# Optimization experiments

Measured on AMD Instinct MI355X. Metric: run time of the kernel, lower is better.

## Reference

```python
import jax, jax.numpy as jnp
import numpy as np
import math

N_HEAD = 16

def _rope_tables(seq, dh, dtype):
    inv_freq = 1.0 / (10000.0 ** (jnp.arange(0, dh, 2, dtype=jnp.float32) / dh))
    angle = jnp.arange(seq, dtype=jnp.float32)[:, None] * inv_freq[None, :]  # [S, dh/2]
    sin = jnp.repeat(jnp.sin(angle), 2, axis=-1).astype(dtype)  # [S, dh]
    cos = jnp.repeat(jnp.cos(angle), 2, axis=-1).astype(dtype)
    return sin, cos

def _rotate_half(x):
    x_even = x[..., ::2]
    x_odd = x[..., 1::2]
    return jnp.stack([-x_odd, x_even], axis=-1).reshape(x.shape)

def _apply_rope(x, sin, cos):
    # x: [B, H, S, dh]; sin/cos: [S, dh]
    return x * cos[None, None] + _rotate_half(x) * sin[None, None]

def setup_inputs() -> dict:
    key = jax.random.key(0)
    ks = jax.random.split(key, 9)
    B, S, D = 2, 2048, 2048
    scale = 1.0 / math.sqrt(D)
    x = jax.random.normal(ks[0], (B, S, D), dtype=jnp.float32)
    wq = jax.random.normal(ks[1], (D, D), dtype=jnp.float32) * scale
    wk = jax.random.normal(ks[2], (D, D), dtype=jnp.float32) * scale
    wv = jax.random.normal(ks[3], (D, D), dtype=jnp.float32) * scale
    wo = jax.random.normal(ks[4], (D, D), dtype=jnp.float32) * scale
    bq = jnp.zeros((D,), jnp.float32)
    bk = jnp.zeros((D,), jnp.float32)
    bv = jnp.zeros((D,), jnp.float32)
    bo = jnp.zeros((D,), jnp.float32)
    # causal mask: True = masked (strict upper triangle)
    mask = jnp.triu(jnp.ones((S, S), dtype=bool), k=1)[None, None]  # [1,1,S,S]
    return {"x": x, "wq": wq, "bq": bq, "wk": wk, "bk": bk, "wv": wv, "bv": bv,
            "wo": wo, "bo": bo, "mask": mask}

def reference(x, wq, bq, wk, bk, wv, bv, wo, bo, mask):
    B, S, D = x.shape
    H = N_HEAD
    dh = D // H
    # projections (torch Linear: x @ W.T + b)
    q = (x @ wq.T + bq).reshape(B, S, H, dh).transpose(0, 2, 1, 3)  # [B,H,S,dh]
    k = (x @ wk.T + bk).reshape(B, S, H, dh).transpose(0, 2, 1, 3)
    v = (x @ wv.T + bv).reshape(B, S, H, dh).transpose(0, 2, 1, 3)
    sin, cos = _rope_tables(S, dh, x.dtype)
    q = _apply_rope(q, sin, cos)
    k = _apply_rope(k, sin, cos)
    scores = jnp.einsum('bhqd,bhkd->bhqk', q, k) / math.sqrt(dh)
    scores = jnp.where(mask, -jnp.inf, scores)
    attn = jax.nn.softmax(scores, axis=-1)
    attn = jnp.nan_to_num(attn, nan=0.0)
    out = jnp.einsum('bhqk,bhkd->bhqd', attn, v)  # [B,H,S,dh]
    out = out.transpose(0, 2, 1, 3).reshape(B, S, D)
    return out @ wo.T + bo
```

## Files before the change

### kernel.cpp

```cpp
#include <hip/hip_runtime.h>
#include <math.h>


typedef _Float16 half8 __attribute__((ext_vector_type(8)));
typedef _Float16 half4v __attribute__((ext_vector_type(4)));
typedef float f32x4 __attribute__((ext_vector_type(4)));

__device__ __forceinline__ void gl_lds16(const void* g, void* l) {
  __builtin_amdgcn_global_load_lds(
      (const __attribute__((address_space(1))) unsigned int*)g,
      (__attribute__((address_space(3))) unsigned int*)l, 16, 0, 0);
}

__global__ void cast_f32_f16(const float* __restrict__ src, _Float16* __restrict__ dst, int n4) {
  int i = blockIdx.x * blockDim.x + threadIdx.x;
  if (i >= n4) return;
  float4 v = reinterpret_cast<const float4*>(src)[i];
  half4v o;
  o[0] = (_Float16)v.x; o[1] = (_Float16)v.y; o[2] = (_Float16)v.z; o[3] = (_Float16)v.w;
  reinterpret_cast<half4v*>(dst)[i] = o;
}

__global__ void cast_w(const float* __restrict__ w0, const float* __restrict__ w1,
                       const float* __restrict__ w2, const float* __restrict__ w3,
                       _Float16* __restrict__ wdst) {
  const float* s = blockIdx.y == 0 ? w0 : blockIdx.y == 1 ? w1 : blockIdx.y == 2 ? w2 : w3;
  int i = blockIdx.x * blockDim.x + threadIdx.x;
  float4 v = reinterpret_cast<const float4*>(s)[i];
  half4v o;
  o[0] = (_Float16)v.x; o[1] = (_Float16)v.y; o[2] = (_Float16)v.z; o[3] = (_Float16)v.w;
  reinterpret_cast<half4v*>(wdst)[(size_t)blockIdx.y * 1048576 + i] = o;
}

template <bool OUT_F32>
__global__ __launch_bounds__(512, 2) void gemm_bt256(
    const _Float16* __restrict__ A,
    const _Float16* __restrict__ B,
    const float* __restrict__ b0, const float* __restrict__ b1,
    const float* __restrict__ b2,
    void* __restrict__ Cout,
    int M, int N, int K) {
  __shared__ _Float16 As[2][16384];
  __shared__ _Float16 Bs[2][16384];
  const int bm = blockIdx.y * 256, bn = blockIdx.x * 256;
  const int tid = threadIdx.x;
  const int wave = tid >> 6, lane = tid & 63;
  const int quad = lane >> 4, l16 = lane & 15;
  const int wm = (wave >> 2) * 128, wn = (wave & 3) * 64;

  const int srow = tid >> 3;
  const int sx = (tid & 7) ^ (srow & 7);
  const _Float16* Ag = A + (size_t)(bm + srow) * K + sx * 8;
  const _Float16* Bg[4];
#pragma unroll
  for (int c = 0; c < 4; ++c) {
    int r = (((c * 2 + (srow >> 5)) & 3) << 6) + ((c >> 1) << 5) + (srow & 31);
    Bg[c] = B + (size_t)(bn + r) * K + sx * 8;
  }

#define STAGE_A(buf, R, kt) \
  gl_lds16(Ag + (size_t)(R) * K + (kt) * 64, &As[buf][(R) * 64 + tid * 8])
#define STAGE_B(buf, c, kt) \
  gl_lds16(Bg[c] + (kt) * 64, &Bs[buf][(c) * 4096 + tid * 8])

  const int axor = l16 & 7;
  const int sl0 = ((0 + quad) ^ axor) * 8;
  const int sl1 = ((4 + quad) ^ axor) * 8;
  const int aoff = (wm + l16) * 64;
  const int q4 = (wn >> 6) * 32;

#define RD_A(i, kk) \
  (*reinterpret_cast<const half8*>(&As[cur][aoff + (i) * 1024 + ((kk) ? sl1 : sl0)]))
#define RD_B(j, kk) \
  (*reinterpret_cast<const half8*>( \
      &Bs[cur][((((j) >> 1) * 128 + q4 + ((j) & 1) * 16 + l16)) * 64 + ((kk) ? sl1 : sl0)]))

  f32x4 acc[8][4];
#pragma unroll
  for (int i = 0; i < 8; ++i)
#pragma unroll
    for (int j = 0; j < 4; ++j) acc[i][j] = f32x4{0.f, 0.f, 0.f, 0.f};

  half8 a[4][2], b[4][2];
  const int NT = K >> 6;

  STAGE_A(0, 0, 0); STAGE_A(0, 128, 0);
  STAGE_B(0, 0, 0); STAGE_B(0, 1, 0);
  STAGE_B(0, 2, 0); STAGE_B(0, 3, 0);
  STAGE_A(0, 64, 0); STAGE_A(0, 192, 0);
  if (NT > 1) {
    STAGE_A(1, 0, 1); STAGE_A(1, 128, 1);
    STAGE_B(1, 0, 1); STAGE_B(1, 1, 1);
    STAGE_B(1, 2, 1); STAGE_B(1, 3, 1);
    asm volatile("s_waitcnt vmcnt(6)");
  } else {
    asm volatile("s_waitcnt vmcnt(0)");
  }
  __builtin_amdgcn_s_barrier();

  for (int t = 0; t < NT; ++t) {
    const int cur = t & 1, nxt = cur ^ 1;
    const bool pf1 = (t + 1 < NT);
    const bool pf2 = (t + 2 < NT);

#pragma unroll
    for (int i = 0; i < 4; ++i) {
      a[i][0] = RD_A(i, 0); a[i][1] = RD_A(i, 1);
    }
#pragma unroll
    for (int j = 0; j < 2; ++j) {
      b[j][0] = RD_B(j, 0); b[j][1] = RD_B(j, 1);
    }
    if (pf1) { STAGE_A(nxt, 64, t + 1); STAGE_A(nxt, 192, t + 1); }
    __builtin_amdgcn_s_barrier();
    __builtin_amdgcn_s_setprio(1);
#pragma unroll
    for (int i = 0; i < 4; ++i)
#pragma unroll
      for (int j = 0; j < 2; ++j) {
        acc[i][j] = __builtin_amdgcn_mfma_f32_16x16x32_f16(a[i][0], b[j][0], acc[i][j], 0, 0, 0);
        acc[i][j] = __builtin_amdgcn_mfma_f32_16x16x32_f16(a[i][1], b[j][1], acc[i][j], 0, 0, 0);
      }
    __builtin_amdgcn_s_setprio(0);
    __builtin_amdgcn_s_barrier();

#pragma unroll
    for (int j = 2; j < 4; ++j) {
      b[j][0] = RD_B(j, 0); b[j][1] = RD_B(j, 1);
    }
    if (pf2) { STAGE_A(cur, 0, t + 2); STAGE_A(cur, 128, t + 2); }
    __builtin_amdgcn_s_barrier();
    __builtin_amdgcn_s_setprio(1);
#pragma unroll
    for (int i = 0; i < 4; ++i)
#pragma unroll
      for (int j = 2; j < 4; ++j) {
        acc[i][j] = __builtin_amdgcn_mfma_f32_16x16x32_f16(a[i][0], b[j][0], acc[i][j], 0, 0, 0);
        acc[i][j] = __builtin_amdgcn_mfma_f32_16x16x32_f16(a[i][1], b[j][1], acc[i][j], 0, 0, 0);
      }
    __builtin_amdgcn_s_setprio(0);
    __builtin_amdgcn_s_barrier();

#pragma unroll
    for (int i = 0; i < 4; ++i) {
      a[i][0] = RD_A(i + 4, 0); a[i][1] = RD_A(i + 4, 1);
    }
    if (pf2) { STAGE_B(cur, 0, t + 2); STAGE_B(cur, 1, t + 2); }
    __builtin_amdgcn_s_barrier();
    __builtin_amdgcn_s_setprio(1);
#pragma unroll
    for (int i = 0; i < 4; ++i)
#pragma unroll
      for (int j = 0; j < 2; ++j) {
        acc[i + 4][j] = __builtin_amdgcn_mfma_f32_16x16x32_f16(a[i][0], b[j][0], acc[i + 4][j], 0, 0, 0);
        acc[i + 4][j] = __builtin_amdgcn_mfma_f32_16x16x32_f16(a[i][1], b[j][1], acc[i + 4][j], 0, 0, 0);
      }
    __builtin_amdgcn_s_setprio(0);
    __builtin_amdgcn_s_barrier();

    if (pf2) { STAGE_B(cur, 2, t + 2); STAGE_B(cur, 3, t + 2); }
    __builtin_amdgcn_s_barrier();
    __builtin_amdgcn_s_setprio(1);
#pragma unroll
    for (int i = 0; i < 4; ++i)
#pragma unroll
      for (int j = 2; j < 4; ++j) {
        acc[i + 4][j] = __builtin_amdgcn_mfma_f32_16x16x32_f16(a[i][0], b[j][0], acc[i + 4][j], 0, 0, 0);
        acc[i + 4][j] = __builtin_amdgcn_mfma_f32_16x16x32_f16(a[i][1], b[j][1], acc[i + 4][j], 0, 0, 0);
      }
    __builtin_amdgcn_s_setprio(0);
    if (pf2)
      asm volatile("s_waitcnt vmcnt(6)");
    else
      asm volatile("s_waitcnt vmcnt(0)");
    __builtin_amdgcn_s_barrier();
  }

#pragma unroll
  for (int j = 0; j < 4; ++j) {
    const int gc = bn + wn + j * 16 + l16;
    const float* bp = (gc < 2048) ? b0 : (gc < 4096 ? b1 : b2);
    const float bz = bp[gc & 2047];
#pragma unroll
    for (int i = 0; i < 8; ++i) {
#pragma unroll
      for (int r = 0; r < 4; ++r) {
        const int gr = bm + wm + i * 16 + quad * 4 + r;
        float v = acc[i][j][r] + bz;
        if (OUT_F32)
          reinterpret_cast<float*>(Cout)[(size_t)gr * N + gc] = v;
        else
          reinterpret_cast<_Float16*>(Cout)[(size_t)gr * N + gc] = (_Float16)v;
      }
    }
  }
#undef STAGE_A
#undef STAGE_B
#undef RD_A
#undef RD_B
}

template <bool OUT_F32>
__global__ __launch_bounds__(512, 2) void gemm_btn128(
    const _Float16* __restrict__ A,
    const _Float16* __restrict__ B,
    const float* __restrict__ bias,
    void* __restrict__ Cout,
    int M, int N, int K) {
  __shared__ _Float16 As[2][16384];
  __shared__ _Float16 Bs[2][8192];
  const int bm = blockIdx.y * 256, bn = blockIdx.x * 128;
  const int tid = threadIdx.x;
  const int wave = tid >> 6, lane = tid & 63;
  const int quad = lane >> 4, l16 = lane & 15;
  const int wm = (wave >> 2) * 128, wq = wave & 3;

  const int srow = tid >> 3;
  const int sx = (tid & 7) ^ (srow & 7);
  const _Float16* Ag = A + (size_t)(bm + srow) * K + sx * 8;
  const _Float16* Bg[2];
#pragma unroll
  for (int c = 0; c < 2; ++c)
    Bg[c] = B + (size_t)(bn + (srow >> 4) * 32 + c * 16 + (srow & 15)) * K + sx * 8;

#define STAGE_A(buf, R, kt) \
  gl_lds16(Ag + (size_t)(R) * K + (kt) * 64, &As[buf][(R) * 64 + tid * 8])
#define STAGE_B(buf, c, kt) \
  gl_lds16(Bg[c] + (kt) * 64, &Bs[buf][(c) * 4096 + tid * 8])

  const int axor = l16 & 7;
  const int sl0 = ((0 + quad) ^ axor) * 8;
  const int sl1 = ((4 + quad) ^ axor) * 8;
  const int aoff = (wm + l16) * 64;

#define RD_A(i, kk) \
  (*reinterpret_cast<const half8*>(&As[cur][aoff + (i) * 1024 + ((kk) ? sl1 : sl0)]))
#define RD_B(j, kk) \
  (*reinterpret_cast<const half8*>( \
      &Bs[cur][((j) * 64 + wq * 16 + l16) * 64 + ((kk) ? sl1 : sl0)]))

  f32x4 acc[8][2];
#pragma unroll
  for (int i = 0; i < 8; ++i)
#pragma unroll
    for (int j = 0; j < 2; ++j) acc[i][j] = f32x4{0.f, 0.f, 0.f, 0.f};

  half8 a[4][2], b[2][2];
  const int NT = K >> 6;

  STAGE_A(0, 0, 0); STAGE_A(0, 128, 0);
  STAGE_B(0, 0, 0); STAGE_B(0, 1, 0);
  STAGE_A(0, 64, 0); STAGE_A(0, 192, 0);
  if (NT > 1) {
    STAGE_A(1, 0, 1); STAGE_A(1, 128, 1);
    STAGE_B(1, 0, 1); STAGE_B(1, 1, 1);
    STAGE_A(1, 64, 1); STAGE_A(1, 192, 1);
    asm volatile("s_waitcnt vmcnt(6)");
  } else {
    asm volatile("s_waitcnt vmcnt(0)");
  }
  __builtin_amdgcn_s_barrier();

  for (int t = 0; t < NT; ++t) {
    const int cur = t & 1;
    const bool pf2 = (t + 2 < NT);

#pragma unroll
    for (int i = 0; i < 4; ++i) {
      a[i][0] = RD_A(i, 0); a[i][1] = RD_A(i, 1);
    }
    b[0][0] = RD_B(0, 0); b[0][1] = RD_B(0, 1);
    __builtin_amdgcn_s_barrier();
    __builtin_amdgcn_s_setprio(1);
#pragma unroll
    for (int i = 0; i < 4; ++i) {
      acc[i][0] = __builtin_amdgcn_mfma_f32_16x16x32_f16(a[i][0], b[0][0], acc[i][0], 0, 0, 0);
      acc[i][0] = __builtin_amdgcn_mfma_f32_16x16x32_f16(a[i][1], b[0][1], acc[i][0], 0, 0, 0);
    }
    __builtin_amdgcn_s_setprio(0);
    __builtin_amdgcn_s_barrier();

    b[1][0] = RD_B(1, 0); b[1][1] = RD_B(1, 1);
    if (pf2) { STAGE_A(cur, 0, t + 2); STAGE_A(cur, 128, t + 2); }
    __builtin_amdgcn_s_barrier();
    __builtin_amdgcn_s_setprio(1);
#pragma unroll
    for (int i = 0; i < 4; ++i) {
      acc[i][1] = __builtin_amdgcn_mfma_f32_16x16x32_f16(a[i][0], b[1][0], acc[i][1], 0, 0, 0);
      acc[i][1] = __builtin_amdgcn_mfma_f32_16x16x32_f16(a[i][1], b[1][1], acc[i][1], 0, 0, 0);
    }
    __builtin_amdgcn_s_setprio(0);
    __builtin_amdgcn_s_barrier();

#pragma unroll
    for (int i = 0; i < 4; ++i) {
      a[i][0] = RD_A(i + 4, 0); a[i][1] = RD_A(i + 4, 1);
    }
    if (pf2) { STAGE_B(cur, 0, t + 2); STAGE_B(cur, 1, t + 2); }
    __builtin_amdgcn_s_barrier();
    __builtin_amdgcn_s_setprio(1);
#pragma unroll
    for (int i = 0; i < 4; ++i) {
      acc[i + 4][0] = __builtin_amdgcn_mfma_f32_16x16x32_f16(a[i][0], b[0][0], acc[i + 4][0], 0, 0, 0);
      acc[i + 4][0] = __builtin_amdgcn_mfma_f32_16x16x32_f16(a[i][1], b[0][1], acc[i + 4][0], 0, 0, 0);
    }
    __builtin_amdgcn_s_setprio(0);
    __builtin_amdgcn_s_barrier();

    if (pf2) { STAGE_A(cur, 64, t + 2); STAGE_A(cur, 192, t + 2); }
    __builtin_amdgcn_s_barrier();
    __builtin_amdgcn_s_setprio(1);
#pragma unroll
    for (int i = 0; i < 4; ++i) {
      acc[i + 4][1] = __builtin_amdgcn_mfma_f32_16x16x32_f16(a[i][0], b[1][0], acc[i + 4][1], 0, 0, 0);
      acc[i + 4][1] = __builtin_amdgcn_mfma_f32_16x16x32_f16(a[i][1], b[1][1], acc[i + 4][1], 0, 0, 0);
    }
    __builtin_amdgcn_s_setprio(0);
    if (pf2)
      asm volatile("s_waitcnt vmcnt(6)");
    else
      asm volatile("s_waitcnt vmcnt(0)");
    __builtin_amdgcn_s_barrier();
  }

#pragma unroll
  for (int j = 0; j < 2; ++j) {
    const int gc = bn + wq * 32 + j * 16 + l16;
    const float bz = bias[gc & 2047];
#pragma unroll
    for (int i = 0; i < 8; ++i) {
#pragma unroll
      for (int r = 0; r < 4; ++r) {
        const int gr = bm + wm + i * 16 + quad * 4 + r;
        float v = acc[i][j][r] + bz;
        if (OUT_F32)
          reinterpret_cast<float*>(Cout)[(size_t)gr * N + gc] = v;
        else
          reinterpret_cast<_Float16*>(Cout)[(size_t)gr * N + gc] = (_Float16)v;
      }
    }
  }
#undef STAGE_A
#undef STAGE_B
#undef RD_A
#undef RD_B
}

__global__ void rope_inplace(_Float16* __restrict__ qkv, int ngroups) {
  int idx = blockIdx.x * blockDim.x + threadIdx.x;
  if (idx >= ngroups) return;
  int m = idx >> 8;
  int g = idx & 255;
  int s = m & 2047;
  const float scale = 0.088388347648318447f;
  size_t base = (size_t)m * 6144 + g * 8;
  half8 qv = *reinterpret_cast<const half8*>(qkv + base);
  half8 kv = *reinterpret_cast<const half8*>(qkv + base + 2048);
  half8 qo, ko;
#pragma unroll
  for (int j = 0; j < 4; ++j) {
    int i = (g * 4 + j) & 63;
    float ang = (float)s * exp2f(-0.2076205059304601f * (float)i);
    float sn, cs;
    __sincosf(ang, &sn, &cs);
    float e = (float)qv[j * 2], o = (float)qv[j * 2 + 1];
    qo[j * 2]     = (_Float16)((e * cs - o * sn) * scale);
    qo[j * 2 + 1] = (_Float16)((o * cs + e * sn) * scale);
    e = (float)kv[j * 2]; o = (float)kv[j * 2 + 1];
    ko[j * 2]     = (_Float16)(e * cs - o * sn);
    ko[j * 2 + 1] = (_Float16)(o * cs + e * sn);
  }
  *reinterpret_cast<half8*>(qkv + base) = qo;
  *reinterpret_cast<half8*>(qkv + base + 2048) = ko;
}

__global__ __launch_bounds__(256) void transpose_v(const _Float16* __restrict__ qkv,
                                                   _Float16* __restrict__ vt) {
  __shared__ _Float16 t[64][72];
  const int s0 = blockIdx.x * 64;
  const int d0 = blockIdx.y * 64;
  const int bh = blockIdx.z;
  const int b = bh >> 4, h = bh & 15;
  const int tid = threadIdx.x;
#pragma unroll
  for (int p = 0; p < 2; ++p) {
    int chunk = p * 256 + tid;
    int r = chunk >> 3, c8 = (chunk & 7) * 8;
    *reinterpret_cast<half8*>(&t[r][c8]) = *reinterpret_cast<const half8*>(
        &qkv[(size_t)(b * 2048 + s0 + r) * 6144 + 4096 + h * 128 + d0 + c8]);
  }
  __syncthreads();
#pragma unroll
  for (int p = 0; p < 2; ++p) {
    int chunk = p * 256 + tid;
    int dr = chunk >> 3, c8 = (chunk & 7) * 8;
    half8 o;
#pragma unroll
    for (int j = 0; j < 8; ++j) o[j] = t[c8 + j][dr];
    *reinterpret_cast<half8*>(&vt[(size_t)(bh * 128 + d0 + dr) * 2048 + s0 + c8]) = o;
  }
}

__global__ __launch_bounds__(256, 2) void attn_kernel(
    const _Float16* __restrict__ QKV,
    const _Float16* __restrict__ VT,
    _Float16* __restrict__ ctx) {
  constexpr int LD = 6144, S = 2048;
  __shared__ _Float16 Ks[2][8192];
  __shared__ _Float16 Vs[2][8192];
  __shared__ _Float16 P[4][16][80];
  const int bid = blockIdx.x;
  const int bh = bid & 31;
  const int idx = (bid >> 5) & 7;
  const int qb = (bid >> 8) ? idx : 15 - idx;
  const int b = bh >> 4, h = bh & 15;
  const int tid = threadIdx.x;
  const int wv = tid >> 6, lane = tid & 63;
  const int quad = lane >> 4, l16 = lane & 15;
  const int q0 = qb * 128 + wv * 16;
  const int NJ = 2 * qb + 2;

  const _Float16* qp0 = QKV + (size_t)(b * S + q0 + l16) * LD + h * 128;
  half8 aq0[4], aq1[4];
#pragma unroll
  for (int ks = 0; ks < 4; ++ks) {
    aq0[ks] = *reinterpret_cast<const half8*>(qp0 + ks * 32 + quad * 8);
    aq1[ks] = *reinterpret_cast<const half8*>(qp0 + (size_t)64 * LD + ks * 32 + quad * 8);
  }

  const _Float16* gk[4];
  const _Float16* gv[4];
  int lofs[4];
#pragma unroll
  for (int p = 0; p < 4; ++p) {
    int c = p * 256 + tid;
    int cs = c ^ ((c >> 3) & 7);
    int cl16 = cs & 15, cqd = (cs >> 4) & 3;
    int cks = (cs >> 6) & 3, cf = cs >> 8;
    gk[p] = QKV + (size_t)(b * S + cf * 16 + cl16) * LD + 2048 + h * 128 + cks * 32 + cqd * 8;
    int ckv = (cs >> 6) & 1, ct = cs >> 7;
    gv[p] = VT + (size_t)(bh * 128 + ct * 16 + cl16) * S + ckv * 32 + cqd * 8;
    lofs[p] = c * 8;
  }

  const int kofs = (l16 >> 3) * 64 + (((l16 & 7) ^ (quad * 2 + (l16 >> 3)))) * 8;

  f32x4 acc0[8], acc1[8];
#pragma unroll
  for (int t = 0; t < 8; ++t) {
    acc0[t] = f32x4{0.f, 0.f, 0.f, 0.f};
    acc1[t] = f32x4{0.f, 0.f, 0.f, 0.f};
  }
  f32x4 lacc0 = f32x4{0.f, 0.f, 0.f, 0.f};
  f32x4 lacc1 = f32x4{0.f, 0.f, 0.f, 0.f};

  half8 ones;
#pragma unroll
  for (int j = 0; j < 8; ++j) ones[j] = (_Float16)1.0f;

#pragma unroll
  for (int p = 0; p < 4; ++p) gl_lds16(gk[p], &Ks[0][lofs[p]]);
#pragma unroll
  for (int p = 0; p < 4; ++p) gl_lds16(gv[p], &Vs[0][lofs[p]]);

  for (int j = 0; j < NJ; ++j) {
    __syncthreads();
    const int cur = j & 1;
    if (j + 1 < NJ) {
      const size_t ko = (size_t)(j + 1) * 64 * LD;
      const int vo = (j + 1) * 64;
#pragma unroll
      for (int p = 0; p < 4; ++p) gl_lds16(gk[p] + ko, &Ks[cur ^ 1][lofs[p]]);
#pragma unroll
      for (int p = 0; p < 4; ++p) gl_lds16(gv[p] + vo, &Vs[cur ^ 1][lofs[p]]);
    }
    const bool h0 = (j < NJ - 1);
    f32x4 sf0[4], sf1[4];
#pragma unroll
    for (int f = 0; f < 4; ++f) {
      sf0[f] = f32x4{0.f, 0.f, 0.f, 0.f};
      sf1[f] = f32x4{0.f, 0.f, 0.f, 0.f};
    }
#pragma unroll
    for (int f = 0; f < 4; ++f)
#pragma unroll
      for (int ks = 0; ks < 4; ++ks) {
        half8 bk = *reinterpret_cast<const half8*>(&Ks[cur][((f * 4 + ks) * 4 + quad) * 128 + kofs]);
        sf0[f] = __builtin_amdgcn_mfma_f32_16x16x32_f16(aq0[ks], bk, sf0[f], 0, 0, 0);
        sf1[f] = __builtin_amdgcn_mfma_f32_16x16x32_f16(aq1[ks], bk, sf1[f], 0, 0, 0);
      }
    if (j == NJ - 2) {
#pragma unroll
      for (int f = 0; f < 4; ++f) {
        const int key = j * 64 + f * 16 + l16;
#pragma unroll
        for (int r = 0; r < 4; ++r)
          sf0[f][r] = (key <= q0 + quad * 4 + r) ? sf0[f][r] : -1e30f;
      }
    }
    if (j == NJ - 1) {
#pragma unroll
      for (int f = 0; f < 4; ++f) {
        const int key = j * 64 + f * 16 + l16;
#pragma unroll
        for (int r = 0; r < 4; ++r)
          sf1[f][r] = (key <= q0 + 64 + quad * 4 + r) ? sf1[f][r] : -1e30f;
      }
    }
    half8 pa0a, pa0b, pa1a, pa1b;
    if (h0) {
#pragma unroll
      for (int f = 0; f < 4; ++f)
#pragma unroll
        for (int r = 0; r < 4; ++r)
          P[wv][quad * 4 + r][f * 16 + l16] = (_Float16)__expf(sf0[f][r] - 5.0f);
      pa0a = *reinterpret_cast<const half8*>(&P[wv][l16][quad * 8]);
      pa0b = *reinterpret_cast<const half8*>(&P[wv][l16][32 + quad * 8]);
    }
#pragma unroll
    for (int f = 0; f < 4; ++f)
#pragma unroll
      for (int r = 0; r < 4; ++r)
        P[wv][quad * 4 + r][f * 16 + l16] = (_Float16)__expf(sf1[f][r] - 5.0f);
    pa1a = *reinterpret_cast<const half8*>(&P[wv][l16][quad * 8]);
    pa1b = *reinterpret_cast<const half8*>(&P[wv][l16][32 + quad * 8]);
#pragma unroll
    for (int t = 0; t < 8; ++t) {
      half8 bv0 = *reinterpret_cast<const half8*>(&Vs[cur][((t * 2 + 0) * 4 + quad) * 128 + kofs]);
      half8 bv1 = *reinterpret_cast<const half8*>(&Vs[cur][((t * 2 + 1) * 4 + quad) * 128 + kofs]);
      if (h0) {
        acc0[t] = __builtin_amdgcn_mfma_f32_16x16x32_f16(pa0a, bv0, acc0[t], 0, 0, 0);
        acc0[t] = __builtin_amdgcn_mfma_f32_16x16x32_f16(pa0b, bv1, acc0[t], 0, 0, 0);
      }
      acc1[t] = __builtin_amdgcn_mfma_f32_16x16x32_f16(pa1a, bv0, acc1[t], 0, 0, 0);
      acc1[t] = __builtin_amdgcn_mfma_f32_16x16x32_f16(pa1b, bv1, acc1[t], 0, 0, 0);
    }
    if (h0) {
      lacc0 = __builtin_amdgcn_mfma_f32_16x16x32_f16(pa0a, ones, lacc0, 0, 0, 0);
      lacc0 = __builtin_amdgcn_mfma_f32_16x16x32_f16(pa0b, ones, lacc0, 0, 0, 0);
    }
    lacc1 = __builtin_amdgcn_mfma_f32_16x16x32_f16(pa1a, ones, lacc1, 0, 0, 0);
    lacc1 = __builtin_amdgcn_mfma_f32_16x16x32_f16(pa1b, ones, lacc1, 0, 0, 0);
  }

  float inv0[4], inv1[4];
#pragma unroll
  for (int r = 0; r < 4; ++r) {
    inv0[r] = 1.0f / lacc0[r];
    inv1[r] = 1.0f / lacc1[r];
  }
#pragma unroll
  for (int t = 0; t < 8; ++t)
#pragma unroll
    for (int r = 0; r < 4; ++r) {
      const int row0 = q0 + quad * 4 + r;
      ctx[(size_t)(b * S + row0) * 2048 + h * 128 + t * 16 + l16] =
          (_Float16)(acc0[t][r] * inv0[r]);
      ctx[(size_t)(b * S + row0 + 64) * 2048 + h * 128 + t * 16 + l16] =
          (_Float16)(acc1[t][r] * inv1[r]);
    }
}

extern "C" void kernel_launch(void* const* d_in, const int* in_sizes, int n_in,
                              void* d_out, int out_size, void* d_ws, size_t ws_size,
                              hipStream_t stream) {
  const float* x  = (const float*)d_in[0];
  const float* wq = (const float*)d_in[1];
  const float* bq = (const float*)d_in[2];
  const float* wk = (const float*)d_in[3];
  const float* bk = (const float*)d_in[4];
  const float* wv = (const float*)d_in[5];
  const float* bv = (const float*)d_in[6];
  const float* wo = (const float*)d_in[7];
  const float* bo = (const float*)d_in[8];

  _Float16* W      = (_Float16*)d_ws;
  _Float16* xh     = W;
  _Float16* wqkvh  = xh + 8388608;
  _Float16* woh    = wqkvh + 12582912;
  _Float16* qkvlin = woh + 4194304;
  _Float16* vT     = xh;
  _Float16* ctx    = wqkvh;

  cast_f32_f16<<<8192, 256, 0, stream>>>(x, xh, 2097152);
  cast_w<<<dim3(4096, 4), 256, 0, stream>>>(wq, wk, wv, wo, wqkvh);

  gemm_bt256<false><<<dim3(24, 16), 512, 0, stream>>>(xh, wqkvh, bq, bk, bv, qkvlin,
                                                      4096, 6144, 2048);

  rope_inplace<<<4096, 256, 0, stream>>>(qkvlin, 1048576);
  transpose_v<<<dim3(32, 2, 32), 256, 0, stream>>>(qkvlin, vT);
  attn_kernel<<<512, 256, 0, stream>>>(qkvlin, vT, ctx);

  gemm_btn128<true><<<dim3(16, 16), 512, 0, stream>>>(ctx, woh, bo, (float*)d_out,
                                                      4096, 2048, 2048);
}
```

Baseline: 432.8 us.

## Fuse RoPE and query scaling into QKV GEMM epilogue, use exp2 softmax

Removes the separate rope_inplace kernel by applying rotary embedding in the QKV GEMM epilogue. Neighbouring even/odd columns are paired through a lane shuffle, and the sin/cos values are advanced across rows by angle-addition recurrences instead of being recomputed each time. The query scale now includes log2(e), so the attention kernel can use exp2f with a matching shift instead of __expf. The P LDS row padding also changes from 80 to 84. This saves a full read and write pass over Q and K, at the cost of extra epilogue arithmetic and some precision drift from the rotation recurrence.

```diff
diff --git a/kernel.cpp b/kernel.cpp
--- a/kernel.cpp
+++ b/kernel.cpp
@@ -32,13 +32,12 @@
   reinterpret_cast<half4v*>(wdst)[(size_t)blockIdx.y * 1048576 + i] = o;
 }
 
-template <bool OUT_F32>
-__global__ __launch_bounds__(512, 2) void gemm_bt256(
+__global__ __launch_bounds__(512, 2) void gemm_qkv(
     const _Float16* __restrict__ A,
     const _Float16* __restrict__ B,
     const float* __restrict__ b0, const float* __restrict__ b1,
     const float* __restrict__ b2,
-    void* __restrict__ Cout,
+    _Float16* __restrict__ Cout,
     int M, int N, int K) {
   __shared__ _Float16 As[2][16384];
   __shared__ _Float16 Bs[2][16384];
@@ -176,22 +175,53 @@
     __builtin_amdgcn_s_barrier();
   }
 
+  const int region = (bn + wn) >> 11;
+  const float qsc = 0.12754113f;
 #pragma unroll
   for (int j = 0; j < 4; ++j) {
     const int gc = bn + wn + j * 16 + l16;
-    const float* bp = (gc < 2048) ? b0 : (gc < 4096 ? b1 : b2);
+    const float* bp = (region == 0) ? b0 : (region == 1 ? b1 : b2);
     const float bz = bp[gc & 2047];
-#pragma unroll
-    for (int i = 0; i < 8; ++i) {
-#pragma unroll
-      for (int r = 0; r < 4; ++r) {
-        const int gr = bm + wm + i * 16 + quad * 4 + r;
-        float v = acc[i][j][r] + bz;
-        if (OUT_F32)
-          reinterpret_cast<float*>(Cout)[(size_t)gr * N + gc] = v;
-        else
-          reinterpret_cast<_Float16*>(Cout)[(size_t)gr * N + gc] = (_Float16)v;
-      }
+    if (region < 2) {
+      const int fi = (gc >> 1) & 63;
+      const float fr = exp2f(-0.2076205059304601f * (float)fi);
+      float c1, s1, c13, s13;
+      __sincosf(fr, &s1, &c1);
+      __sincosf(13.0f * fr, &s13, &c13);
+      const float sc = (region == 0) ? qsc : 1.0f;
+      const int s0 = (bm + wm + quad * 4) & 2047;
+      float cb, sb;
+      __sincosf((float)s0 * fr, &sb, &cb);
+      cb *= sc; sb *= sc;
+      const bool isodd = (gc & 1) != 0;
+#pragma unroll
+      for (int i = 0; i < 8; ++i) {
+#pragma unroll
+        for (int r = 0; r < 4; ++r) {
+          const int gr = bm + wm + i * 16 + quad * 4 + r;
+          float v = acc[i][j][r] + bz;
+          const float p = __shfl_xor(v, 1);
+          float out = isodd ? (v * cb + p * sb) : (v * cb - p * sb);
+          Cout[(size_t)gr * N + gc] = (_Float16)out;
+          if (!(i == 7 && r == 3)) {
+            if (r < 3) {
+              float cn = cb * c1 - sb * s1;
+              sb = sb * c1 + cb * s1; cb = cn;
+            } else {
+              float cn = cb * c13 - sb * s13;
+              sb = sb * c13 + cb * s13; cb = cn;
+            }
+          }
+        }
+      }
+    } else {
+#pragma unroll
+      for (int i = 0; i < 8; ++i)
+#pragma unroll
+        for (int r = 0; r < 4; ++r) {
+          const int gr = bm + wm + i * 16 + quad * 4 + r;
+          Cout[(size_t)gr * N + gc] = (_Float16)(acc[i][j][r] + bz);
+        }
     }
   }
 #undef STAGE_A
@@ -200,12 +230,11 @@
 #undef RD_B
 }
 
-template <bool OUT_F32>
-__global__ __launch_bounds__(512, 2) void gemm_btn128(
+__global__ __launch_bounds__(512, 2) void gemm_out(
     const _Float16* __restrict__ A,
     const _Float16* __restrict__ B,
     const float* __restrict__ bias,
-    void* __restrict__ Cout,
+    float* __restrict__ Cout,
     int M, int N, int K) {
   __shared__ _Float16 As[2][16384];
   __shared__ _Float16 Bs[2][8192];
@@ -332,11 +361,7 @@
 #pragma unroll
       for (int r = 0; r < 4; ++r) {
         const int gr = bm + wm + i * 16 + quad * 4 + r;
-        float v = acc[i][j][r] + bz;
-        if (OUT_F32)
-          reinterpret_cast<float*>(Cout)[(size_t)gr * N + gc] = v;
-        else
-          reinterpret_cast<_Float16*>(Cout)[(size_t)gr * N + gc] = (_Float16)v;
+        Cout[(size_t)gr * N + gc] = acc[i][j][r] + bz;
       }
     }
   }
@@ -344,34 +369,6 @@
 #undef STAGE_B
 #undef RD_A
 #undef RD_B
-}
-
-__global__ void rope_inplace(_Float16* __restrict__ qkv, int ngroups) {
-  int idx = blockIdx.x * blockDim.x + threadIdx.x;
-  if (idx >= ngroups) return;
-  int m = idx >> 8;
-  int g = idx & 255;
-  int s = m & 2047;
-  const float scale = 0.088388347648318447f;
-  size_t base = (size_t)m * 6144 + g * 8;
-  half8 qv = *reinterpret_cast<const half8*>(qkv + base);
-  half8 kv = *reinterpret_cast<const half8*>(qkv + base + 2048);
-  half8 qo, ko;
-#pragma unroll
-  for (int j = 0; j < 4; ++j) {
-    int i = (g * 4 + j) & 63;
-    float ang = (float)s * exp2f(-0.2076205059304601f * (float)i);
-    float sn, cs;
-    __sincosf(ang, &sn, &cs);
-    float e = (float)qv[j * 2], o = (float)qv[j * 2 + 1];
-    qo[j * 2]     = (_Float16)((e * cs - o * sn) * scale);
-    qo[j * 2 + 1] = (_Float16)((o * cs + e * sn) * scale);
-    e = (float)kv[j * 2]; o = (float)kv[j * 2 + 1];
-    ko[j * 2]     = (_Float16)(e * cs - o * sn);
-    ko[j * 2 + 1] = (_Float16)(o * cs + e * sn);
-  }
-  *reinterpret_cast<half8*>(qkv + base) = qo;
-  *reinterpret_cast<half8*>(qkv + base + 2048) = ko;
 }
 
 __global__ __launch_bounds__(256) void transpose_v(const _Float16* __restrict__ qkv,
@@ -408,7 +405,7 @@
   constexpr int LD = 6144, S = 2048;
   __shared__ _Float16 Ks[2][8192];
   __shared__ _Float16 Vs[2][8192];
-  __shared__ _Float16 P[4][16][80];
+  __shared__ _Float16 P[4][16][84];
   const int bid = blockIdx.x;
   const int bh = bid & 31;
   const int idx = (bid >> 5) & 7;
@@ -419,6 +416,7 @@
   const int quad = lane >> 4, l16 = lane & 15;
   const int q0 = qb * 128 + wv * 16;
   const int NJ = 2 * qb + 2;
+  const float SH = 7.2134752044448169f;
 
   const _Float16* qp0 = QKV + (size_t)(b * S + q0 + l16) * LD + h * 128;
   half8 aq0[4], aq1[4];
@@ -513,7 +511,7 @@
       for (int f = 0; f < 4; ++f)
 #pragma unroll
         for (int r = 0; r < 4; ++r)
-          P[wv][quad * 4 + r][f * 16 + l16] = (_Float16)__expf(sf0[f][r] - 5.0f);
+          P[wv][quad * 4 + r][f * 16 + l16] = (_Float16)exp2f(sf0[f][r] - SH);
       pa0a = *reinterpret_cast<const half8*>(&P[wv][l16][quad * 8]);
       pa0b = *reinterpret_cast<const half8*>(&P[wv][l16][32 + quad * 8]);
     }
@@ -521,7 +519,7 @@
     for (int f = 0; f < 4; ++f)
 #pragma unroll
       for (int r = 0; r < 4; ++r)
-        P[wv][quad * 4 + r][f * 16 + l16] = (_Float16)__expf(sf1[f][r] - 5.0f);
+        P[wv][quad * 4 + r][f * 16 + l16] = (_Float16)exp2f(sf1[f][r] - SH);
     pa1a = *reinterpret_cast<const half8*>(&P[wv][l16][quad * 8]);
     pa1b = *reinterpret_cast<const half8*>(&P[wv][l16][32 + quad * 8]);
 #pragma unroll
@@ -585,13 +583,12 @@
   cast_f32_f16<<<8192, 256, 0, stream>>>(x, xh, 2097152);
   cast_w<<<dim3(4096, 4), 256, 0, stream>>>(wq, wk, wv, wo, wqkvh);
 
-  gemm_bt256<false><<<dim3(24, 16), 512, 0, stream>>>(xh, wqkvh, bq, bk, bv, qkvlin,
-                                                      4096, 6144, 2048);
-
-  rope_inplace<<<4096, 256, 0, stream>>>(qkvlin, 1048576);
+  gemm_qkv<<<dim3(24, 16), 512, 0, stream>>>(xh, wqkvh, bq, bk, bv, qkvlin,
+                                             4096, 6144, 2048);
+
   transpose_v<<<dim3(32, 2, 32), 256, 0, stream>>>(qkvlin, vT);
   attn_kernel<<<512, 256, 0, stream>>>(qkvlin, vT, ctx);
 
-  gemm_btn128<true><<<dim3(16, 16), 512, 0, stream>>>(ctx, woh, bo, (float*)d_out,
-                                                      4096, 2048, 2048);
-}
+  gemm_out<<<dim3(16, 16), 512, 0, stream>>>(ctx, woh, bo, (float*)d_out,
+                                             4096, 2048, 2048);
+}
```

New measurement: 458.8 us. +6.0%, slower.
